# Performance work log

Hardware: AMD Instinct MI355X
Metric: run time of the kernel (lower is better)

The kernel has to match this reference:

```python
import jax, jax.numpy as jnp
import numpy as np

L = 8          # n_layer
D = 512        # hidden_size
DIN = 1024     # d_inner = 2*D (Mamba expand=2)
DS = 16        # d_state
DTR = 32       # dt_rank = ceil(D/16)
K = 4          # d_conv
NACT = 3       # n_action_to_predict
ADIM = 4
LOSS_COEF = 1.0

def silu(x):
    return x * jax.nn.sigmoid(x)

def rms(x, w, eps=1e-5):
    return x * jax.lax.rsqrt(jnp.mean(x * x, axis=-1, keepdims=True) + eps) * w

def tokenize(images, states, actions, patch_w, patch_b, state_w, state_b, act_w, act_b):
    # images [b,l,3,224,224] -> 14x14 patches of 3*16*16=768 -> mean-pooled image token
    b, l = images.shape[:2]
    p = images.reshape(b, l, 3, 14, 16, 14, 16).transpose(0, 1, 3, 5, 2, 4, 6).reshape(b, l, 196, 768)
    img = jnp.mean(p @ patch_w.T + patch_b, axis=2)            # [b,l,D] token_type 1
    st = states[:, :, 0] @ state_w.T + state_b                 # [b,l,D] token_type 2
    ac = actions[:, :, :NACT - 1] @ act_w.T + act_b            # [b,l,NACT-1,D] token_type 3
    toks = jnp.concatenate([img[:, :, None], st[:, :, None], ac], axis=2)  # [b,l,1+NACT,D]
    return toks.reshape(b, l * (1 + NACT), D)

def mamba_mixer(x, in_w, cw, cb, xpw, dtw, dtb, alog, dp, ow):
    # x: [b,S,D]
    b, S, _ = x.shape
    xz = x @ in_w.T                                   # [b,S,2*DIN]
    xi, z = xz[..., :DIN], xz[..., DIN:]
    # causal depthwise conv, kernel K
    xp = jnp.pad(xi, ((0, 0), (K - 1, 0), (0, 0)))
    xc = cb + sum(cw[:, k] * xp[:, k:k + S, :] for k in range(K))
    xc = silu(xc)
    proj = xc @ xpw.T                                  # [b,S,DTR+2*DS]
    dtr, Bm, Cm = proj[..., :DTR], proj[..., DTR:DTR + DS], proj[..., DTR + DS:]
    dt = jax.nn.softplus(dtr @ dtw.T + dtb)            # [b,S,DIN]
    A = -jnp.exp(alog)                                 # [DIN,DS]
    dA = jnp.exp(dt[..., None] * A)                    # [b,S,DIN,DS]
    dBx = dt[..., None] * Bm[:, :, None, :] * xc[..., None]
    def step(h, inp):
        a_t, bx_t = inp
        h = a_t * h + bx_t
        return h, h
    _, hs = jax.lax.scan(step, jnp.zeros((b, DIN, DS), x.dtype),
                         (dA.swapaxes(0, 1), dBx.swapaxes(0, 1)))  # hs [S,b,DIN,DS]
    y = jnp.einsum('sbdn,bsn->bsd', hs, Cm) + dp * xc
    return (y * silu(z)) @ ow.T

def _forward(images, seq_length, states, actions, action_labels,
             patch_w, patch_b, state_w, state_b, act_w, act_b,
             norm1_w, in_proj_w, conv_w, conv_b, x_proj_w, dt_w, dt_b,
             A_log, Dp, out_proj_w, norm2_w, fc1_w, fc2_w, norm_f_w,
             head_w, head_b):
    b, l = images.shape[:2]
    hidden = tokenize(images, states, actions, patch_w, patch_b, state_w, state_b, act_w, act_b)
    residual = jnp.zeros_like(hidden)
    for i in range(L):
        residual = hidden + residual
        hidden = mamba_mixer(rms(residual, norm1_w[i]), in_proj_w[i], conv_w[i], conv_b[i],
                             x_proj_w[i], dt_w[i], dt_b[i], A_log[i], Dp[i], out_proj_w[i])
        residual = hidden + residual
        g = rms(residual, norm2_w[i]) @ fc1_w[i].T       # GatedMLP fc1 -> [.., 2*DIN]
        hidden = (g[..., :DIN] * silu(g[..., DIN:])) @ fc2_w[i].T
    residual = hidden + residual
    hidden = rms(residual, norm_f_w)
    # static action-token positions: per-frame tokens [img, state, act, act] -> indices 1..3
    hs = hidden.reshape(b, l, 1 + NACT, D)[:, :, 1:, :]
    action_preds = hs @ head_w.T + head_b                # [b,l,NACT,ADIM]
    mask = (jnp.arange(l)[None, :] < seq_length[:, None]).astype(jnp.float32)
    la = jnp.mean(jnp.abs(action_preds - action_labels), axis=(2, 3))
    la = (la * mask).sum(axis=1) / jnp.clip(mask.sum(axis=1), 1.0)
    loss = jnp.mean(la) * LOSS_COEF
    return loss, action_preds

def setup_inputs() -> dict:
    key = jax.random.key(0)
    ks = iter(jax.random.split(key, 40))
    nrm = lambda shape, s=0.02: s * jax.random.normal(next(ks), shape, dtype=jnp.float32)
    inp = {
        'images': jax.random.normal(next(ks), (2, 64, 3, 224, 224), jnp.float32),
        'seq_length': jax.random.randint(next(ks), (2,), 1, 65),
        'states': jax.random.normal(next(ks), (2, 64, NACT, 7), jnp.float32),
        'actions': jax.random.normal(next(ks), (2, 64, NACT, ADIM), jnp.float32),
        'action_labels': jax.random.normal(next(ks), (2, 64, NACT, ADIM), jnp.float32),
        'patch_w': nrm((D, 768)), 'patch_b': jnp.zeros((D,), jnp.float32),
        'state_w': nrm((D, 7)), 'state_b': jnp.zeros((D,), jnp.float32),
        'act_w': nrm((D, ADIM)), 'act_b': jnp.zeros((D,), jnp.float32),
        'norm1_w': jnp.ones((L, D), jnp.float32),
        'in_proj_w': nrm((L, 2 * DIN, D)),
        'conv_w': nrm((L, DIN, K), 0.1), 'conv_b': jnp.zeros((L, DIN), jnp.float32),
        'x_proj_w': nrm((L, DTR + 2 * DS, DIN)),
        'dt_w': nrm((L, DIN, DTR)), 'dt_b': jnp.full((L, DIN), -4.6, jnp.float32),
        'A_log': jnp.log(jnp.broadcast_to(jnp.arange(1, DS + 1, dtype=jnp.float32), (L, DIN, DS))).copy(),
        'Dp': jnp.ones((L, DIN), jnp.float32),
        'out_proj_w': nrm((L, D, DIN)),
        'norm2_w': jnp.ones((L, D), jnp.float32),
        'fc1_w': nrm((L, 2 * DIN, D)), 'fc2_w': nrm((L, D, DIN)),
        'norm_f_w': jnp.ones((D,), jnp.float32),
        'head_w': nrm((ADIM, D)), 'head_b': jnp.zeros((ADIM,), jnp.float32),
    }
    return inp

def reference(images, seq_length, states, actions, action_labels,
              patch_w, patch_b, state_w, state_b, act_w, act_b,
              norm1_w, in_proj_w, conv_w, conv_b, x_proj_w, dt_w, dt_b,
              A_log, Dp, out_proj_w, norm2_w, fc1_w, fc2_w, norm_f_w,
              head_w, head_b):
    return _forward(images, seq_length, states, actions, action_labels,
                    patch_w, patch_b, state_w, state_b, act_w, act_b,
                    norm1_w, in_proj_w, conv_w, conv_b, x_proj_w, dt_w, dt_b,
                    A_log, Dp, out_proj_w, norm2_w, fc1_w, fc2_w, norm_f_w,
                    head_w, head_b)
```

## Files before the change

### kernel.cpp

```cpp
#include <hip/hip_runtime.h>


#define NTOK 512
#define SEQ  256
#define CS   32
#define NC   8

typedef __attribute__((ext_vector_type(8))) short bf16x8;
typedef __attribute__((ext_vector_type(16))) float f32x16;

__device__ __forceinline__ float silu_f(float x) { return x / (1.0f + expf(-x)); }
__device__ __forceinline__ float softplus_f(float x) {
  return (x > 20.0f) ? x : log1pf(expf(x));
}

__device__ __forceinline__ void split_pack(float4 v, uint2* hi, uint2* lo) {
  uint ux = __float_as_uint(v.x), uy = __float_as_uint(v.y);
  uint uz = __float_as_uint(v.z), uw = __float_as_uint(v.w);
  hi->x = (ux >> 16) | (uy & 0xffff0000u);
  hi->y = (uz >> 16) | (uw & 0xffff0000u);
  float lx = v.x - __uint_as_float(ux & 0xffff0000u);
  float ly = v.y - __uint_as_float(uy & 0xffff0000u);
  float lz = v.z - __uint_as_float(uz & 0xffff0000u);
  float lw = v.w - __uint_as_float(uw & 0xffff0000u);
  lo->x = (__float_as_uint(lx) >> 16) | (__float_as_uint(ly) & 0xffff0000u);
  lo->y = (__float_as_uint(lz) >> 16) | (__float_as_uint(lw) & 0xffff0000u);
}

__global__ __launch_bounds__(256) void gemm_bs_k(const float* __restrict__ A,
                                                 const float* __restrict__ B,
                                                 float* __restrict__ C,
                                                 int M, int N, int K, int Kc) {
  __shared__ alignas(16) ushort sAh[2][2][2][512];
  __shared__ alignas(16) ushort sAl[2][2][2][512];
  __shared__ alignas(16) ushort sBh[2][2][2][512];
  __shared__ alignas(16) ushort sBl[2][2][2][512];
  int t = threadIdx.x;
  int bn = blockIdx.x, bm = blockIdx.y, z = blockIdx.z;
  const float* Ab = A + (size_t)bm * 64 * K + (size_t)z * Kc;
  const float* Bb = B + (size_t)bn * 64 * K + (size_t)z * Kc;
  float* Cb = C + (size_t)z * M * N;
  int r = t >> 2, kc = (t & 3) << 2;
  int st = r >> 5, m = r & 31;
  int off = ((kc >> 3) << 8) + (m << 3) + (kc & 7);
  int w = t >> 6, lane = t & 63;
  int wr = w >> 1, wc = w & 1;

  f32x16 acc;
#pragma unroll
  for (int i = 0; i < 16; ++i) acc[i] = 0.f;

  int ns = Kc >> 5;
  const float* Ar = Ab + (size_t)r * K + kc;
  const float* Br = Bb + (size_t)r * K + kc;
  float4 a0 = *(const float4*)&Ar[0];
  float4 a1 = *(const float4*)&Ar[16];
  float4 b0 = *(const float4*)&Br[0];
  float4 b1 = *(const float4*)&Br[16];
  {
    uint2 hi, lo;
    split_pack(a0, &hi, &lo);
    *(uint2*)&sAh[0][0][st][off] = hi; *(uint2*)&sAl[0][0][st][off] = lo;
    split_pack(a1, &hi, &lo);
    *(uint2*)&sAh[0][1][st][off] = hi; *(uint2*)&sAl[0][1][st][off] = lo;
    split_pack(b0, &hi, &lo);
    *(uint2*)&sBh[0][0][st][off] = hi; *(uint2*)&sBl[0][0][st][off] = lo;
    split_pack(b1, &hi, &lo);
    *(uint2*)&sBh[0][1][st][off] = hi; *(uint2*)&sBl[0][1][st][off] = lo;
  }
  __syncthreads();
  for (int ssi = 0; ssi < ns; ++ssi) {
    int buf = ssi & 1;
    if (ssi + 1 < ns) {
      a0 = *(const float4*)&Ar[(ssi + 1) * 32];
      a1 = *(const float4*)&Ar[(ssi + 1) * 32 + 16];
      b0 = *(const float4*)&Br[(ssi + 1) * 32];
      b1 = *(const float4*)&Br[(ssi + 1) * 32 + 16];
    }
    bf16x8 ah = *(bf16x8*)&sAh[buf][0][wr][lane << 3];
    bf16x8 al = *(bf16x8*)&sAl[buf][0][wr][lane << 3];
    bf16x8 bh = *(bf16x8*)&sBh[buf][0][wc][lane << 3];
    bf16x8 bl = *(bf16x8*)&sBl[buf][0][wc][lane << 3];
    acc = __builtin_amdgcn_mfma_f32_32x32x16_bf16(ah, bh, acc, 0, 0, 0);
    acc = __builtin_amdgcn_mfma_f32_32x32x16_bf16(al, bh, acc, 0, 0, 0);
    acc = __builtin_amdgcn_mfma_f32_32x32x16_bf16(ah, bl, acc, 0, 0, 0);
    bf16x8 ah1 = *(bf16x8*)&sAh[buf][1][wr][lane << 3];
    bf16x8 al1 = *(bf16x8*)&sAl[buf][1][wr][lane << 3];
    bf16x8 bh1 = *(bf16x8*)&sBh[buf][1][wc][lane << 3];
    bf16x8 bl1 = *(bf16x8*)&sBl[buf][1][wc][lane << 3];
    acc = __builtin_amdgcn_mfma_f32_32x32x16_bf16(ah1, bh1, acc, 0, 0, 0);
    acc = __builtin_amdgcn_mfma_f32_32x32x16_bf16(al1, bh1, acc, 0, 0, 0);
    acc = __builtin_amdgcn_mfma_f32_32x32x16_bf16(ah1, bl1, acc, 0, 0, 0);
    if (ssi + 1 < ns) {
      uint2 hi, lo;
      split_pack(a0, &hi, &lo);
      *(uint2*)&sAh[buf ^ 1][0][st][off] = hi; *(uint2*)&sAl[buf ^ 1][0][st][off] = lo;
      split_pack(a1, &hi, &lo);
      *(uint2*)&sAh[buf ^ 1][1][st][off] = hi; *(uint2*)&sAl[buf ^ 1][1][st][off] = lo;
      split_pack(b0, &hi, &lo);
      *(uint2*)&sBh[buf ^ 1][0][st][off] = hi; *(uint2*)&sBl[buf ^ 1][0][st][off] = lo;
      split_pack(b1, &hi, &lo);
      *(uint2*)&sBh[buf ^ 1][1][st][off] = hi; *(uint2*)&sBl[buf ^ 1][1][st][off] = lo;
    }
    __syncthreads();
  }
  int col = lane & 31, rq = lane >> 5;
  float* Cw = Cb + (size_t)(bm * 64 + wr * 32) * N + bn * 64 + wc * 32 + col;
#pragma unroll
  for (int rg = 0; rg < 16; ++rg) {
    int row = (rg & 3) + ((rg >> 2) << 3) + (rq << 2);
    Cw[(size_t)row * N] = acc[rg];
  }
}

__global__ __launch_bounds__(256) void gemm_glu_k(const float* __restrict__ G,
                                                  const float* __restrict__ B,
                                                  float* __restrict__ C,
                                                  int M, int N, int K, int Kc) {
  __shared__ alignas(16) ushort sAh[2][2][2][512];
  __shared__ alignas(16) ushort sAl[2][2][2][512];
  __shared__ alignas(16) ushort sBh[2][2][2][512];
  __shared__ alignas(16) ushort sBl[2][2][2][512];
  int t = threadIdx.x;
  int bn = blockIdx.x, bm = blockIdx.y, z = blockIdx.z;
  const float* Gb = G + (size_t)bm * 64 * 2048 + (size_t)z * Kc;
  const float* Bb = B + (size_t)bn * 64 * K + (size_t)z * Kc;
  float* Cb = C + (size_t)z * M * N;
  int r = t >> 2, kc = (t & 3) << 2;
  int st = r >> 5, m = r & 31;
  int off = ((kc >> 3) << 8) + (m << 3) + (kc & 7);
  int w = t >> 6, lane = t & 63;
  int wr = w >> 1, wc = w & 1;

  f32x16 acc;
#pragma unroll
  for (int i = 0; i < 16; ++i) acc[i] = 0.f;

  int ns = Kc >> 5;
  const float* gr = Gb + (size_t)r * 2048 + kc;
  const float* Br = Bb + (size_t)r * K + kc;
  float4 ga0 = *(const float4*)&gr[0];
  float4 gz0 = *(const float4*)&gr[1024];
  float4 ga1 = *(const float4*)&gr[16];
  float4 gz1 = *(const float4*)&gr[1040];
  float4 b0 = *(const float4*)&Br[0];
  float4 b1 = *(const float4*)&Br[16];
  {
    float4 a0 = {ga0.x * silu_f(gz0.x), ga0.y * silu_f(gz0.y),
                 ga0.z * silu_f(gz0.z), ga0.w * silu_f(gz0.w)};
    float4 a1 = {ga1.x * silu_f(gz1.x), ga1.y * silu_f(gz1.y),
                 ga1.z * silu_f(gz1.z), ga1.w * silu_f(gz1.w)};
    uint2 hi, lo;
    split_pack(a0, &hi, &lo);
    *(uint2*)&sAh[0][0][st][off] = hi; *(uint2*)&sAl[0][0][st][off] = lo;
    split_pack(a1, &hi, &lo);
    *(uint2*)&sAh[0][1][st][off] = hi; *(uint2*)&sAl[0][1][st][off] = lo;
    split_pack(b0, &hi, &lo);
    *(uint2*)&sBh[0][0][st][off] = hi; *(uint2*)&sBl[0][0][st][off] = lo;
    split_pack(b1, &hi, &lo);
    *(uint2*)&sBh[0][1][st][off] = hi; *(uint2*)&sBl[0][1][st][off] = lo;
  }
  __syncthreads();
  for (int ssi = 0; ssi < ns; ++ssi) {
    int buf = ssi & 1;
    if (ssi + 1 < ns) {
      ga0 = *(const float4*)&gr[(ssi + 1) * 32];
      gz0 = *(const float4*)&gr[1024 + (ssi + 1) * 32];
      ga1 = *(const float4*)&gr[(ssi + 1) * 32 + 16];
      gz1 = *(const float4*)&gr[1040 + (ssi + 1) * 32];
      b0 = *(const float4*)&Br[(ssi + 1) * 32];
      b1 = *(const float4*)&Br[(ssi + 1) * 32 + 16];
    }
    bf16x8 ah = *(bf16x8*)&sAh[buf][0][wr][lane << 3];
    bf16x8 al = *(bf16x8*)&sAl[buf][0][wr][lane << 3];
    bf16x8 bh = *(bf16x8*)&sBh[buf][0][wc][lane << 3];
    bf16x8 bl = *(bf16x8*)&sBl[buf][0][wc][lane << 3];
    acc = __builtin_amdgcn_mfma_f32_32x32x16_bf16(ah, bh, acc, 0, 0, 0);
    acc = __builtin_amdgcn_mfma_f32_32x32x16_bf16(al, bh, acc, 0, 0, 0);
    acc = __builtin_amdgcn_mfma_f32_32x32x16_bf16(ah, bl, acc, 0, 0, 0);
    bf16x8 ah1 = *(bf16x8*)&sAh[buf][1][wr][lane << 3];
    bf16x8 al1 = *(bf16x8*)&sAl[buf][1][wr][lane << 3];
    bf16x8 bh1 = *(bf16x8*)&sBh[buf][1][wc][lane << 3];
    bf16x8 bl1 = *(bf16x8*)&sBl[buf][1][wc][lane << 3];
    acc = __builtin_amdgcn_mfma_f32_32x32x16_bf16(ah1, bh1, acc, 0, 0, 0);
    acc = __builtin_amdgcn_mfma_f32_32x32x16_bf16(al1, bh1, acc, 0, 0, 0);
    acc = __builtin_amdgcn_mfma_f32_32x32x16_bf16(ah1, bl1, acc, 0, 0, 0);
    if (ssi + 1 < ns) {
      float4 a0 = {ga0.x * silu_f(gz0.x), ga0.y * silu_f(gz0.y),
                   ga0.z * silu_f(gz0.z), ga0.w * silu_f(gz0.w)};
      float4 a1 = {ga1.x * silu_f(gz1.x), ga1.y * silu_f(gz1.y),
                   ga1.z * silu_f(gz1.z), ga1.w * silu_f(gz1.w)};
      uint2 hi, lo;
      split_pack(a0, &hi, &lo);
      *(uint2*)&sAh[buf ^ 1][0][st][off] = hi; *(uint2*)&sAl[buf ^ 1][0][st][off] = lo;
      split_pack(a1, &hi, &lo);
      *(uint2*)&sAh[buf ^ 1][1][st][off] = hi; *(uint2*)&sAl[buf ^ 1][1][st][off] = lo;
      split_pack(b0, &hi, &lo);
      *(uint2*)&sBh[buf ^ 1][0][st][off] = hi; *(uint2*)&sBl[buf ^ 1][0][st][off] = lo;
      split_pack(b1, &hi, &lo);
      *(uint2*)&sBh[buf ^ 1][1][st][off] = hi; *(uint2*)&sBl[buf ^ 1][1][st][off] = lo;
    }
    __syncthreads();
  }
  int col = lane & 31, rq = lane >> 5;
  float* Cw = Cb + (size_t)(bm * 64 + wr * 32) * N + bn * 64 + wc * 32 + col;
#pragma unroll
  for (int rg = 0; rg < 16; ++rg) {
    int row = (rg & 3) + ((rg >> 2) << 3) + (rq << 2);
    Cw[(size_t)row * N] = acc[rg];
  }
}

__global__ void patch_part_k(const float* __restrict__ img, float* __restrict__ pmp) {
  int blk = blockIdx.x;
  int bl = blk / 14, hb = blk % 14;
  int t = threadIdx.x;
  int c = t >> 6, hi = (t >> 2) & 15, wi4 = t & 3;
  const float* base = img + (size_t)bl * 3 * 50176 + (size_t)c * 50176 +
                      (size_t)(hb * 16 + hi) * 224 + wi4 * 4;
  float4 s = {0.f, 0.f, 0.f, 0.f};
#pragma unroll
  for (int wb = 0; wb < 14; ++wb) {
    float4 v = *(const float4*)&base[wb * 16];
    s.x += v.x; s.y += v.y; s.z += v.z; s.w += v.w;
  }
  ((float4*)(pmp + (size_t)blk * 768))[t] = s;
}

__global__ void patch_red_k(const float* __restrict__ pmp, float* __restrict__ meanp) {
  int bl = blockIdx.x;
  int t = threadIdx.x;
  float4 s = {0.f, 0.f, 0.f, 0.f};
  for (int hb = 0; hb < 14; ++hb) {
    float4 v = ((const float4*)(pmp + (size_t)(bl * 14 + hb) * 768))[t];
    s.x += v.x; s.y += v.y; s.z += v.z; s.w += v.w;
  }
  const float inv = 1.0f / 196.0f;
  float4 o = {s.x * inv, s.y * inv, s.z * inv, s.w * inv};
  ((float4*)(meanp + (size_t)bl * 768))[t] = o;
}

__global__ void tokenize_k(const float* __restrict__ imgp,
                           const float* __restrict__ states,
                           const float* __restrict__ actions,
                           const float* __restrict__ pb,
                           const float* __restrict__ sw, const float* __restrict__ sb,
                           const float* __restrict__ aw, const float* __restrict__ ab,
                           float* __restrict__ hidden, float* __restrict__ residual) {
  int tok = blockIdx.x;
  int t = threadIdx.x;
  int j = tok & 3;
  int bl = tok >> 2;
  int o0 = t * 4;
  float out[4];
  if (j == 0) {
    float4 a = ((const float4*)pb)[t];
    const float* ip = imgp + (size_t)bl * 512;
#pragma unroll
    for (int p = 0; p < 8; ++p) {
      float4 v = ((const float4*)(ip + (size_t)p * 65536))[t];
      a.x += v.x; a.y += v.y; a.z += v.z; a.w += v.w;
    }
    out[0] = a.x; out[1] = a.y; out[2] = a.z; out[3] = a.w;
  } else if (j == 1) {
    const float* sv = states + (size_t)bl * 21;
#pragma unroll
    for (int i = 0; i < 4; ++i) {
      int o = o0 + i;
      float acc = sb[o];
      for (int k = 0; k < 7; ++k) acc += sw[o * 7 + k] * sv[k];
      out[i] = acc;
    }
  } else {
    const float* av = actions + ((size_t)bl * 3 + (j - 2)) * 4;
#pragma unroll
    for (int i = 0; i < 4; ++i) {
      int o = o0 + i;
      float acc = ab[o];
      for (int k = 0; k < 4; ++k) acc += aw[o * 4 + k] * av[k];
      out[i] = acc;
    }
  }
  float4 ov = {out[0], out[1], out[2], out[3]};
  ((float4*)(hidden + (size_t)tok * 512))[t] = ov;
  float4 z4 = {0.f, 0.f, 0.f, 0.f};
  ((float4*)(residual + (size_t)tok * 512))[t] = z4;
}

__global__ void addnorm_k(const float* __restrict__ hid, int parts,
                          float* __restrict__ res,
                          const float* __restrict__ w, float* __restrict__ xn) {
  int tok = blockIdx.x;
  int t = threadIdx.x;
  float4* r4 = (float4*)(res + (size_t)tok * 512);
  float4 r = r4[t];
  const float4* hp = (const float4*)(hid + (size_t)tok * 512);
  for (int p = 0; p < parts; ++p) {
    float4 h = hp[t];
    r.x += h.x; r.y += h.y; r.z += h.z; r.w += h.w;
    hp += 65536;
  }
  r4[t] = r;
  float ss = r.x * r.x + r.y * r.y + r.z * r.z + r.w * r.w;
  for (int off = 32; off; off >>= 1) ss += __shfl_down(ss, off, 64);
  __shared__ float s2[2];
  if ((t & 63) == 0) s2[t >> 6] = ss;
  __syncthreads();
  float tot = s2[0] + s2[1];
  float scale = rsqrtf(tot * (1.0f / 512.0f) + 1e-5f);
  float4 wv = ((const float4*)w)[t];
  float4 o = {r.x * scale * wv.x, r.y * scale * wv.y,
              r.z * scale * wv.z, r.w * scale * wv.w};
  ((float4*)(xn + (size_t)tok * 512))[t] = o;
}

__global__ __launch_bounds__(256) void convproj_k(const float* __restrict__ xz,
                                                  const float* __restrict__ cw,
                                                  const float* __restrict__ cb,
                                                  const float* __restrict__ xpw,
                                                  const float* __restrict__ dtw,
                                                  const float* __restrict__ dtbias,
                                                  float* __restrict__ xc,
                                                  float* __restrict__ proj,
                                                  float* __restrict__ dt) {
  int tok = blockIdx.x;
  int t = threadIdx.x;
  int b = tok >> 8, s = tok & 255;
  __shared__ float xr[1024];
  __shared__ float pp[4][64];
  __shared__ float pr[64];
  int d4 = t * 4;
  float4 cw0 = ((const float4*)cw)[d4];
  float4 cw1 = ((const float4*)cw)[d4 + 1];
  float4 cw2 = ((const float4*)cw)[d4 + 2];
  float4 cw3 = ((const float4*)cw)[d4 + 3];
  float acc0 = cb[d4], acc1 = cb[d4 + 1], acc2 = cb[d4 + 2], acc3 = cb[d4 + 3];
  const float* base = xz + (size_t)b * 256 * 2048 + d4;
  const float wk0[4] = {cw0.x, cw0.y, cw0.z, cw0.w};
  const float wk1[4] = {cw1.x, cw1.y, cw1.z, cw1.w};
  const float wk2[4] = {cw2.x, cw2.y, cw2.z, cw2.w};
  const float wk3[4] = {cw3.x, cw3.y, cw3.z, cw3.w};
#pragma unroll
  for (int k = 0; k < 4; ++k) {
    int row = s + k - 3;
    if (row >= 0) {
      float4 v = *(const float4*)&base[(size_t)row * 2048];
      acc0 += wk0[k] * v.x; acc1 += wk1[k] * v.y;
      acc2 += wk2[k] * v.z; acc3 += wk3[k] * v.w;
    }
  }
  float4 xc4 = {silu_f(acc0), silu_f(acc1), silu_f(acc2), silu_f(acc3)};
  ((float4*)(xc + (size_t)tok * 1024))[t] = xc4;
  *(float4*)&xr[d4] = xc4;
  __syncthreads();
  int n = t & 63, q = t >> 6;
  {
    const float* wrow = xpw + (size_t)n * 1024 + q * 256;
    const float* xq = xr + q * 256;
    float acc = 0.f;
    for (int k = 0; k < 256; k += 4)
      acc += wrow[k] * xq[k] + wrow[k + 1] * xq[k + 1] +
             wrow[k + 2] * xq[k + 2] + wrow[k + 3] * xq[k + 3];
    pp[q][n] = acc;
  }
  __syncthreads();
  if (t < 64) {
    float v = pp[0][t] + pp[1][t] + pp[2][t] + pp[3][t];
    pr[t] = v;
    proj[(size_t)tok * 64 + t] = v;
  }
  __syncthreads();
#pragma unroll
  for (int i = 0; i < 4; ++i) {
    int d = t * 4 + i;
    const float* dw = dtw + (size_t)d * 32;
    float a = dtbias[d];
    for (int k = 0; k < 32; ++k) a += dw[k] * pr[k];
    dt[(size_t)tok * 1024 + d] = softplus_f(a);
  }
}

__global__ __launch_bounds__(512) void scan_k(const float* __restrict__ dt,
                                              const float* __restrict__ proj,
                                              const float* __restrict__ xc,
                                              const float* __restrict__ xz,
                                              const float* __restrict__ alog,
                                              const float* __restrict__ Dp,
                                              float* __restrict__ yz) {
  __shared__ float sDt[256][4];
  __shared__ float sXc[256][4];
  __shared__ float sZ[256][4];
  __shared__ float sBC[256][32];
  __shared__ float2 sP[8][4][16];
  __shared__ float sY[256][4];
  int t = threadIdx.x;
  int g = blockIdx.x;
  int b = g >> 8;
  int d0 = (g & 255) << 2;
  int c = t >> 6, dl = (t >> 4) & 3, n = t & 15;
  int d = d0 + dl;
  const float* dtb = dt + (size_t)b * 256 * 1024 + d0;
  const float* xcb = xc + (size_t)b * 256 * 1024 + d0;
  const float* zb  = xz + (size_t)b * 256 * 2048 + 1024 + d0;
  const float* pbp = proj + (size_t)b * 256 * 64 + 32;
  float* yb = yz + (size_t)b * 256 * 1024 + d0;

  if (t < 256) {
    *(float4*)&sDt[t][0] = *(const float4*)&dtb[(size_t)t * 1024];
    *(float4*)&sZ[t][0]  = *(const float4*)&zb[(size_t)t * 2048];
  } else {
    int u = t - 256;
    *(float4*)&sXc[u][0] = *(const float4*)&xcb[(size_t)u * 1024];
  }
#pragma unroll
  for (int i = 0; i < 4; ++i) {
    int idx = i * 512 + t;
    int s = idx >> 3, c4 = (idx & 7) << 2;
    *(float4*)&sBC[s][c4] = *(const float4*)&pbp[(size_t)s * 64 + c4];
  }
  float A = -expf(alog[d * 16 + n]);
  float dp = Dp[d];
  __syncthreads();

  float Ap = 1.f, Bacc = 0.f;
#pragma unroll
  for (int i = 0; i < CS; ++i) {
    int s = (c << 5) + i;
    float dtv = sDt[s][dl];
    float dA = __expf(dtv * A);
    Bacc = dA * Bacc + dtv * sBC[s][n] * sXc[s][dl];
    Ap *= dA;
  }
  sP[c][dl][n] = make_float2(Ap, Bacc);
  __syncthreads();

  float h = 0.f;
  for (int cc = 0; cc < c; ++cc) {
    float2 p = sP[cc][dl][n];
    h = p.x * h + p.y;
  }

#pragma unroll
  for (int i = 0; i < CS; ++i) {
    int s = (c << 5) + i;
    float dtv = sDt[s][dl];
    float xcv = sXc[s][dl];
    float dA = __expf(dtv * A);
    h = dA * h + dtv * sBC[s][n] * xcv;
    float yc = h * sBC[s][16 + n];
    yc += __shfl_xor(yc, 1, 64);
    yc += __shfl_xor(yc, 2, 64);
    yc += __shfl_xor(yc, 4, 64);
    yc += __shfl_xor(yc, 8, 64);
    if (n == 0) sY[s][dl] = (yc + dp * xcv) * silu_f(sZ[s][dl]);
  }
  __syncthreads();
  if (t < 256)
    *(float4*)&yb[(size_t)t * 1024] = *(const float4*)&sY[t][0];
}

__global__ void head_k(const float* __restrict__ hf, const float* __restrict__ hw,
                       const float* __restrict__ hb, const float* __restrict__ labels,
                       float* __restrict__ preds, float* __restrict__ labs) {
  int blk = blockIdx.x;
  int j = blk % 3;
  int l = (blk / 3) % 64;
  int b = blk / 192;
  int row = b * 256 + l * 4 + 1 + j;
  int t = threadIdx.x;
  const float* x = hf + (size_t)row * 512;
  float acc[4] = {0.f, 0.f, 0.f, 0.f};
  for (int k = t; k < 512; k += 64) {
    float xv = x[k];
#pragma unroll
    for (int a = 0; a < 4; ++a) acc[a] += xv * hw[a * 512 + k];
  }
  for (int off = 32; off; off >>= 1) {
#pragma unroll
    for (int a = 0; a < 4; ++a) acc[a] += __shfl_down(acc[a], off, 64);
  }
  if (t == 0) {
    const float* lab = labels + (size_t)blk * 4;
    float sd = 0.f;
#pragma unroll
    for (int a = 0; a < 4; ++a) {
      float p = acc[a] + hb[a];
      preds[(size_t)blk * 4 + a] = p;
      sd += fabsf(p - lab[a]);
    }
    labs[blk] = sd;
  }
}

__global__ void loss_k(const float* __restrict__ labs, const int* __restrict__ seqlen,
                       float* __restrict__ out) {
  int t = threadIdx.x;
  int b = t >> 6, l = t & 63;
  float la = (labs[(b * 64 + l) * 3] + labs[(b * 64 + l) * 3 + 1] +
              labs[(b * 64 + l) * 3 + 2]) * (1.0f / 12.0f);
  float m = (l < seqlen[b]) ? 1.f : 0.f;
  float v = la * m;
  for (int off = 32; off; off >>= 1) {
    v += __shfl_down(v, off, 64);
    m += __shfl_down(m, off, 64);
  }
  __shared__ float sb_[2];
  if ((t & 63) == 0) sb_[b] = v / fmaxf(m, 1.0f);
  __syncthreads();
  if (t == 0) out[0] = 0.5f * (sb_[0] + sb_[1]);
}

extern "C" void kernel_launch(void* const* d_in, const int* in_sizes, int n_in,
                              void* d_out, int out_size, void* d_ws, size_t ws_size,
                              hipStream_t stream) {
  const float* images     = (const float*)d_in[0];
  const int*   seq_length = (const int*)d_in[1];
  const float* states     = (const float*)d_in[2];
  const float* actions    = (const float*)d_in[3];
  const float* labels     = (const float*)d_in[4];
  const float* patch_w    = (const float*)d_in[5];
  const float* patch_b    = (const float*)d_in[6];
  const float* state_w    = (const float*)d_in[7];
  const float* state_b    = (const float*)d_in[8];
  const float* act_w      = (const float*)d_in[9];
  const float* act_b      = (const float*)d_in[10];
  const float* norm1_w    = (const float*)d_in[11];
  const float* in_proj_w  = (const float*)d_in[12];
  const float* conv_w     = (const float*)d_in[13];
  const float* conv_b     = (const float*)d_in[14];
  const float* x_proj_w   = (const float*)d_in[15];
  const float* dt_w       = (const float*)d_in[16];
  const float* dt_b       = (const float*)d_in[17];
  const float* A_log      = (const float*)d_in[18];
  const float* Dp         = (const float*)d_in[19];
  const float* out_proj_w = (const float*)d_in[20];
  const float* norm2_w    = (const float*)d_in[21];
  const float* fc1_w      = (const float*)d_in[22];
  const float* fc2_w      = (const float*)d_in[23];
  const float* norm_f_w   = (const float*)d_in[24];
  const float* head_w     = (const float*)d_in[25];
  const float* head_b     = (const float*)d_in[26];

  float* out = (float*)d_out;

  float* ws = (float*)d_ws;
  float* meanp    = ws; ws += 98304;
  float* hidden   = ws; ws += 262144;
  float* residual = ws; ws += 262144;
  float* xn       = ws; ws += 262144;
  float* xz       = ws; ws += 1048576;
  float* xc       = ws; ws += 524288;
  float* proj     = ws; ws += 32768;
  float* dtbuf    = ws; ws += 524288;
  float* yz       = ws; ws += 524288;
  float* labs     = ws; ws += 384;
  float* cpart    = ws; ws += 1048576;
  float* pmp      = ws; ws += 1376256;

  hipLaunchKernelGGL(patch_part_k, dim3(1792), dim3(192), 0, stream, images, pmp);
  hipLaunchKernelGGL(patch_red_k, dim3(128), dim3(192), 0, stream, pmp, meanp);
  hipLaunchKernelGGL(gemm_bs_k, dim3(8, 2, 8), dim3(256), 0, stream,
                     meanp, patch_w, cpart, 128, 512, 768, 96);
  hipLaunchKernelGGL(tokenize_k, dim3(512), dim3(128), 0, stream, cpart, states, actions,
                     patch_b, state_w, state_b, act_w, act_b, hidden, residual);

  for (int i = 0; i < 8; ++i) {
    const float* n1 = norm1_w + i * 512;
    const float* ipw = in_proj_w + (size_t)i * 2048 * 512;
    const float* cw = conv_w + (size_t)i * 4096;
    const float* cb = conv_b + (size_t)i * 1024;
    const float* xpw = x_proj_w + (size_t)i * 65536;
    const float* dtw = dt_w + (size_t)i * 32768;
    const float* dtbias = dt_b + (size_t)i * 1024;
    const float* al = A_log + (size_t)i * 16384;
    const float* dpp = Dp + (size_t)i * 1024;
    const float* opw = out_proj_w + (size_t)i * 524288;
    const float* n2 = norm2_w + i * 512;
    const float* f1 = fc1_w + (size_t)i * 1048576;
    const float* f2 = fc2_w + (size_t)i * 524288;

    if (i == 0)
      hipLaunchKernelGGL(addnorm_k, dim3(512), dim3(128), 0, stream,
                         hidden, 1, residual, n1, xn);
    else
      hipLaunchKernelGGL(addnorm_k, dim3(512), dim3(128), 0, stream,
                         cpart, 4, residual, n1, xn);
    hipLaunchKernelGGL(gemm_bs_k, dim3(32, 8, 1), dim3(256), 0, stream,
                       xn, ipw, xz, 512, 2048, 512, 512);
    hipLaunchKernelGGL(convproj_k, dim3(512), dim3(256), 0, stream,
                       xz, cw, cb, xpw, dtw, dtbias, xc, proj, dtbuf);
    hipLaunchKernelGGL(scan_k, dim3(512), dim3(512), 0, stream,
                       dtbuf, proj, xc, xz, al, dpp, yz);
    hipLaunchKernelGGL(gemm_bs_k, dim3(8, 8, 4), dim3(256), 0, stream,
                       yz, opw, cpart, 512, 512, 1024, 256);
    hipLaunchKernelGGL(addnorm_k, dim3(512), dim3(128), 0, stream,
                       cpart, 4, residual, n2, xn);
    hipLaunchKernelGGL(gemm_bs_k, dim3(32, 8, 1), dim3(256), 0, stream,
                       xn, f1, xz, 512, 2048, 512, 512);
    hipLaunchKernelGGL(gemm_glu_k, dim3(8, 8, 4), dim3(256), 0, stream,
                       xz, f2, cpart, 512, 512, 1024, 256);
  }

  hipLaunchKernelGGL(addnorm_k, dim3(512), dim3(128), 0, stream,
                     cpart, 4, residual, norm_f_w, xn);
  hipLaunchKernelGGL(head_k, dim3(384), dim3(64), 0, stream, xn, head_w, head_b, labels,
                     out + 1, labs);
  hipLaunchKernelGGL(loss_k, dim3(1), dim3(128), 0, stream, labs, seq_length, out);
}
```

Baseline: 1.117 ms.

## Fuse RMSNorm into GEMM prologues and residual add into GEMM epilogues

Removes the standalone addnorm kernels. The in_proj and fc1 GEMMs now compute each row's RMS scale from the residual themselves and apply the norm weight while staging tiles. The out_proj and fc2 GEMMs drop split-K and add their results directly into the residual buffer. Patch pooling collapses into one kernel, and the final norm folds into the head kernel. This cuts launches and intermediate traffic, but the RMW GEMMs now launch only 64 blocks with serial K, which lowers parallelism, and every norm-fused GEMM block recomputes the row norm.

```diff
diff --git a/kernel.cpp b/kernel.cpp
--- a/kernel.cpp
+++ b/kernel.cpp
@@ -4,7 +4,6 @@
 #define NTOK 512
 #define SEQ  256
 #define CS   32
-#define NC   8
 
 typedef __attribute__((ext_vector_type(8))) short bf16x8;
 typedef __attribute__((ext_vector_type(16))) float f32x16;
@@ -113,19 +112,126 @@
   }
 }
 
-__global__ __launch_bounds__(256) void gemm_glu_k(const float* __restrict__ G,
-                                                  const float* __restrict__ B,
-                                                  float* __restrict__ C,
-                                                  int M, int N, int K, int Kc) {
+__global__ __launch_bounds__(256) void gemm_an_k(const float* __restrict__ res,
+                                                 const float* __restrict__ nw,
+                                                 const float* __restrict__ B,
+                                                 float* __restrict__ C, int N) {
   __shared__ alignas(16) ushort sAh[2][2][2][512];
   __shared__ alignas(16) ushort sAl[2][2][2][512];
   __shared__ alignas(16) ushort sBh[2][2][2][512];
   __shared__ alignas(16) ushort sBl[2][2][2][512];
-  int t = threadIdx.x;
-  int bn = blockIdx.x, bm = blockIdx.y, z = blockIdx.z;
-  const float* Gb = G + (size_t)bm * 64 * 2048 + (size_t)z * Kc;
-  const float* Bb = B + (size_t)bn * 64 * K + (size_t)z * Kc;
-  float* Cb = C + (size_t)z * M * N;
+  __shared__ float snw[512];
+  int t = threadIdx.x;
+  int bn = blockIdx.x, bm = blockIdx.y;
+  int r = t >> 2, kc = (t & 3) << 2;
+  int row = bm * 64 + r;
+  int st = r >> 5, m = r & 31;
+  int off = ((kc >> 3) << 8) + (m << 3) + (kc & 7);
+  int w = t >> 6, lane = t & 63;
+  int wr = w >> 1, wc = w & 1;
+
+  if (t < 128) *(float4*)&snw[t * 4] = *(const float4*)&nw[t * 4];
+
+  const float* rp = res + (size_t)row * 512;
+  float ss = 0.f;
+#pragma unroll 8
+  for (int j = 0; j < 32; ++j) {
+    float4 v = *(const float4*)&rp[((t & 3) << 2) + j * 16];
+    ss += v.x * v.x + v.y * v.y + v.z * v.z + v.w * v.w;
+  }
+  ss += __shfl_xor(ss, 1, 64);
+  ss += __shfl_xor(ss, 2, 64);
+  float scale = rsqrtf(ss * (1.0f / 512.0f) + 1e-5f);
+  __syncthreads();
+
+  f32x16 acc;
+#pragma unroll
+  for (int i = 0; i < 16; ++i) acc[i] = 0.f;
+
+  const float* Ar = rp + kc;
+  const float* Br = B + (size_t)(bn * 64 + r) * 512 + kc;
+  float4 a0 = *(const float4*)&Ar[0];
+  float4 a1 = *(const float4*)&Ar[16];
+  float4 b0 = *(const float4*)&Br[0];
+  float4 b1 = *(const float4*)&Br[16];
+  {
+    float4 w0 = *(const float4*)&snw[kc];
+    float4 w1 = *(const float4*)&snw[kc + 16];
+    float4 p0 = {a0.x * scale * w0.x, a0.y * scale * w0.y,
+                 a0.z * scale * w0.z, a0.w * scale * w0.w};
+    float4 p1 = {a1.x * scale * w1.x, a1.y * scale * w1.y,
+                 a1.z * scale * w1.z, a1.w * scale * w1.w};
+    uint2 hi, lo;
+    split_pack(p0, &hi, &lo);
+    *(uint2*)&sAh[0][0][st][off] = hi; *(uint2*)&sAl[0][0][st][off] = lo;
+    split_pack(p1, &hi, &lo);
+    *(uint2*)&sAh[0][1][st][off] = hi; *(uint2*)&sAl[0][1][st][off] = lo;
+    split_pack(b0, &hi, &lo);
+    *(uint2*)&sBh[0][0][st][off] = hi; *(uint2*)&sBl[0][0][st][off] = lo;
+    split_pack(b1, &hi, &lo);
+    *(uint2*)&sBh[0][1][st][off] = hi; *(uint2*)&sBl[0][1][st][off] = lo;
+  }
+  __syncthreads();
+  for (int ssi = 0; ssi < 16; ++ssi) {
+    int buf = ssi & 1;
+    if (ssi + 1 < 16) {
+      a0 = *(const float4*)&Ar[(ssi + 1) * 32];
+      a1 = *(const float4*)&Ar[(ssi + 1) * 32 + 16];
+      b0 = *(const float4*)&Br[(ssi + 1) * 32];
+      b1 = *(const float4*)&Br[(ssi + 1) * 32 + 16];
+    }
+    bf16x8 ah = *(bf16x8*)&sAh[buf][0][wr][lane << 3];
+    bf16x8 al = *(bf16x8*)&sAl[buf][0][wr][lane << 3];
+    bf16x8 bh = *(bf16x8*)&sBh[buf][0][wc][lane << 3];
+    bf16x8 bl = *(bf16x8*)&sBl[buf][0][wc][lane << 3];
+    acc = __builtin_amdgcn_mfma_f32_32x32x16_bf16(ah, bh, acc, 0, 0, 0);
+    acc = __builtin_amdgcn_mfma_f32_32x32x16_bf16(al, bh, acc, 0, 0, 0);
+    acc = __builtin_amdgcn_mfma_f32_32x32x16_bf16(ah, bl, acc, 0, 0, 0);
+    bf16x8 ah1 = *(bf16x8*)&sAh[buf][1][wr][lane << 3];
+    bf16x8 al1 = *(bf16x8*)&sAl[buf][1][wr][lane << 3];
+    bf16x8 bh1 = *(bf16x8*)&sBh[buf][1][wc][lane << 3];
+    bf16x8 bl1 = *(bf16x8*)&sBl[buf][1][wc][lane << 3];
+    acc = __builtin_amdgcn_mfma_f32_32x32x16_bf16(ah1, bh1, acc, 0, 0, 0);
+    acc = __builtin_amdgcn_mfma_f32_32x32x16_bf16(al1, bh1, acc, 0, 0, 0);
+    acc = __builtin_amdgcn_mfma_f32_32x32x16_bf16(ah1, bl1, acc, 0, 0, 0);
+    if (ssi + 1 < 16) {
+      int c0 = (ssi + 1) * 32 + kc;
+      float4 w0 = *(const float4*)&snw[c0];
+      float4 w1 = *(const float4*)&snw[c0 + 16];
+      float4 p0 = {a0.x * scale * w0.x, a0.y * scale * w0.y,
+                   a0.z * scale * w0.z, a0.w * scale * w0.w};
+      float4 p1 = {a1.x * scale * w1.x, a1.y * scale * w1.y,
+                   a1.z * scale * w1.z, a1.w * scale * w1.w};
+      uint2 hi, lo;
+      split_pack(p0, &hi, &lo);
+      *(uint2*)&sAh[buf ^ 1][0][st][off] = hi; *(uint2*)&sAl[buf ^ 1][0][st][off] = lo;
+      split_pack(p1, &hi, &lo);
+      *(uint2*)&sAh[buf ^ 1][1][st][off] = hi; *(uint2*)&sAl[buf ^ 1][1][st][off] = lo;
+      split_pack(b0, &hi, &lo);
+      *(uint2*)&sBh[buf ^ 1][0][st][off] = hi; *(uint2*)&sBl[buf ^ 1][0][st][off] = lo;
+      split_pack(b1, &hi, &lo);
+      *(uint2*)&sBh[buf ^ 1][1][st][off] = hi; *(uint2*)&sBl[buf ^ 1][1][st][off] = lo;
+    }
+    __syncthreads();
+  }
+  int col = lane & 31, rq = lane >> 5;
+  float* Cw = C + (size_t)(bm * 64 + wr * 32) * N + bn * 64 + wc * 32 + col;
+#pragma unroll
+  for (int rg = 0; rg < 16; ++rg) {
+    int row2 = (rg & 3) + ((rg >> 2) << 3) + (rq << 2);
+    Cw[(size_t)row2 * N] = acc[rg];
+  }
+}
+
+__global__ __launch_bounds__(256) void gemm_rmw_k(const float* __restrict__ A,
+                                                  const float* __restrict__ B,
+                                                  float* __restrict__ resid) {
+  __shared__ alignas(16) ushort sAh[2][2][2][512];
+  __shared__ alignas(16) ushort sAl[2][2][2][512];
+  __shared__ alignas(16) ushort sBh[2][2][2][512];
+  __shared__ alignas(16) ushort sBl[2][2][2][512];
+  int t = threadIdx.x;
+  int bn = blockIdx.x, bm = blockIdx.y;
   int r = t >> 2, kc = (t & 3) << 2;
   int st = r >> 5, m = r & 31;
   int off = ((kc >> 3) << 8) + (m << 3) + (kc & 7);
@@ -136,9 +242,89 @@
 #pragma unroll
   for (int i = 0; i < 16; ++i) acc[i] = 0.f;
 
-  int ns = Kc >> 5;
-  const float* gr = Gb + (size_t)r * 2048 + kc;
-  const float* Br = Bb + (size_t)r * K + kc;
+  const float* Ar = A + (size_t)(bm * 64 + r) * 1024 + kc;
+  const float* Br = B + (size_t)(bn * 64 + r) * 1024 + kc;
+  float4 a0 = *(const float4*)&Ar[0];
+  float4 a1 = *(const float4*)&Ar[16];
+  float4 b0 = *(const float4*)&Br[0];
+  float4 b1 = *(const float4*)&Br[16];
+  {
+    uint2 hi, lo;
+    split_pack(a0, &hi, &lo);
+    *(uint2*)&sAh[0][0][st][off] = hi; *(uint2*)&sAl[0][0][st][off] = lo;
+    split_pack(a1, &hi, &lo);
+    *(uint2*)&sAh[0][1][st][off] = hi; *(uint2*)&sAl[0][1][st][off] = lo;
+    split_pack(b0, &hi, &lo);
+    *(uint2*)&sBh[0][0][st][off] = hi; *(uint2*)&sBl[0][0][st][off] = lo;
+    split_pack(b1, &hi, &lo);
+    *(uint2*)&sBh[0][1][st][off] = hi; *(uint2*)&sBl[0][1][st][off] = lo;
+  }
+  __syncthreads();
+  for (int ssi = 0; ssi < 32; ++ssi) {
+    int buf = ssi & 1;
+    if (ssi + 1 < 32) {
+      a0 = *(const float4*)&Ar[(ssi + 1) * 32];
+      a1 = *(const float4*)&Ar[(ssi + 1) * 32 + 16];
+      b0 = *(const float4*)&Br[(ssi + 1) * 32];
+      b1 = *(const float4*)&Br[(ssi + 1) * 32 + 16];
+    }
+    bf16x8 ah = *(bf16x8*)&sAh[buf][0][wr][lane << 3];
+    bf16x8 al = *(bf16x8*)&sAl[buf][0][wr][lane << 3];
+    bf16x8 bh = *(bf16x8*)&sBh[buf][0][wc][lane << 3];
+    bf16x8 bl = *(bf16x8*)&sBl[buf][0][wc][lane << 3];
+    acc = __builtin_amdgcn_mfma_f32_32x32x16_bf16(ah, bh, acc, 0, 0, 0);
+    acc = __builtin_amdgcn_mfma_f32_32x32x16_bf16(al, bh, acc, 0, 0, 0);
+    acc = __builtin_amdgcn_mfma_f32_32x32x16_bf16(ah, bl, acc, 0, 0, 0);
+    bf16x8 ah1 = *(bf16x8*)&sAh[buf][1][wr][lane << 3];
+    bf16x8 al1 = *(bf16x8*)&sAl[buf][1][wr][lane << 3];
+    bf16x8 bh1 = *(bf16x8*)&sBh[buf][1][wc][lane << 3];
+    bf16x8 bl1 = *(bf16x8*)&sBl[buf][1][wc][lane << 3];
+    acc = __builtin_amdgcn_mfma_f32_32x32x16_bf16(ah1, bh1, acc, 0, 0, 0);
+    acc = __builtin_amdgcn_mfma_f32_32x32x16_bf16(al1, bh1, acc, 0, 0, 0);
+    acc = __builtin_amdgcn_mfma_f32_32x32x16_bf16(ah1, bl1, acc, 0, 0, 0);
+    if (ssi + 1 < 32) {
+      uint2 hi, lo;
+      split_pack(a0, &hi, &lo);
+      *(uint2*)&sAh[buf ^ 1][0][st][off] = hi; *(uint2*)&sAl[buf ^ 1][0][st][off] = lo;
+      split_pack(a1, &hi, &lo);
+      *(uint2*)&sAh[buf ^ 1][1][st][off] = hi; *(uint2*)&sAl[buf ^ 1][1][st][off] = lo;
+      split_pack(b0, &hi, &lo);
+      *(uint2*)&sBh[buf ^ 1][0][st][off] = hi; *(uint2*)&sBl[buf ^ 1][0][st][off] = lo;
+      split_pack(b1, &hi, &lo);
+      *(uint2*)&sBh[buf ^ 1][1][st][off] = hi; *(uint2*)&sBl[buf ^ 1][1][st][off] = lo;
+    }
+    __syncthreads();
+  }
+  int col = lane & 31, rq = lane >> 5;
+  float* Cw = resid + (size_t)(bm * 64 + wr * 32) * 512 + bn * 64 + wc * 32 + col;
+#pragma unroll
+  for (int rg = 0; rg < 16; ++rg) {
+    int row = (rg & 3) + ((rg >> 2) << 3) + (rq << 2);
+    Cw[(size_t)row * 512] += acc[rg];
+  }
+}
+
+__global__ __launch_bounds__(256) void gemm_glu_rmw_k(const float* __restrict__ G,
+                                                      const float* __restrict__ B,
+                                                      float* __restrict__ resid) {
+  __shared__ alignas(16) ushort sAh[2][2][2][512];
+  __shared__ alignas(16) ushort sAl[2][2][2][512];
+  __shared__ alignas(16) ushort sBh[2][2][2][512];
+  __shared__ alignas(16) ushort sBl[2][2][2][512];
+  int t = threadIdx.x;
+  int bn = blockIdx.x, bm = blockIdx.y;
+  int r = t >> 2, kc = (t & 3) << 2;
+  int st = r >> 5, m = r & 31;
+  int off = ((kc >> 3) << 8) + (m << 3) + (kc & 7);
+  int w = t >> 6, lane = t & 63;
+  int wr = w >> 1, wc = w & 1;
+
+  f32x16 acc;
+#pragma unroll
+  for (int i = 0; i < 16; ++i) acc[i] = 0.f;
+
+  const float* gr = G + (size_t)(bm * 64 + r) * 2048 + kc;
+  const float* Br = B + (size_t)(bn * 64 + r) * 1024 + kc;
   float4 ga0 = *(const float4*)&gr[0];
   float4 gz0 = *(const float4*)&gr[1024];
   float4 ga1 = *(const float4*)&gr[16];
@@ -161,9 +347,9 @@
     *(uint2*)&sBh[0][1][st][off] = hi; *(uint2*)&sBl[0][1][st][off] = lo;
   }
   __syncthreads();
-  for (int ssi = 0; ssi < ns; ++ssi) {
+  for (int ssi = 0; ssi < 32; ++ssi) {
     int buf = ssi & 1;
-    if (ssi + 1 < ns) {
+    if (ssi + 1 < 32) {
       ga0 = *(const float4*)&gr[(ssi + 1) * 32];
       gz0 = *(const float4*)&gr[1024 + (ssi + 1) * 32];
       ga1 = *(const float4*)&gr[(ssi + 1) * 32 + 16];
@@ -185,7 +371,7 @@
     acc = __builtin_amdgcn_mfma_f32_32x32x16_bf16(ah1, bh1, acc, 0, 0, 0);
     acc = __builtin_amdgcn_mfma_f32_32x32x16_bf16(al1, bh1, acc, 0, 0, 0);
     acc = __builtin_amdgcn_mfma_f32_32x32x16_bf16(ah1, bl1, acc, 0, 0, 0);
-    if (ssi + 1 < ns) {
+    if (ssi + 1 < 32) {
       float4 a0 = {ga0.x * silu_f(gz0.x), ga0.y * silu_f(gz0.y),
                    ga0.z * silu_f(gz0.z), ga0.w * silu_f(gz0.w)};
       float4 a1 = {ga1.x * silu_f(gz1.x), ga1.y * silu_f(gz1.y),
@@ -203,37 +389,28 @@
     __syncthreads();
   }
   int col = lane & 31, rq = lane >> 5;
-  float* Cw = Cb + (size_t)(bm * 64 + wr * 32) * N + bn * 64 + wc * 32 + col;
+  float* Cw = resid + (size_t)(bm * 64 + wr * 32) * 512 + bn * 64 + wc * 32 + col;
 #pragma unroll
   for (int rg = 0; rg < 16; ++rg) {
     int row = (rg & 3) + ((rg >> 2) << 3) + (rq << 2);
-    Cw[(size_t)row * N] = acc[rg];
-  }
-}
-
-__global__ void patch_part_k(const float* __restrict__ img, float* __restrict__ pmp) {
-  int blk = blockIdx.x;
-  int bl = blk / 14, hb = blk % 14;
+    Cw[(size_t)row * 512] += acc[rg];
+  }
+}
+
+__global__ void patch_k(const float* __restrict__ img, float* __restrict__ meanp) {
+  int bl = blockIdx.x;
   int t = threadIdx.x;
   int c = t >> 6, hi = (t >> 2) & 15, wi4 = t & 3;
-  const float* base = img + (size_t)bl * 3 * 50176 + (size_t)c * 50176 +
-                      (size_t)(hb * 16 + hi) * 224 + wi4 * 4;
-  float4 s = {0.f, 0.f, 0.f, 0.f};
-#pragma unroll
-  for (int wb = 0; wb < 14; ++wb) {
-    float4 v = *(const float4*)&base[wb * 16];
-    s.x += v.x; s.y += v.y; s.z += v.z; s.w += v.w;
-  }
-  ((float4*)(pmp + (size_t)blk * 768))[t] = s;
-}
-
-__global__ void patch_red_k(const float* __restrict__ pmp, float* __restrict__ meanp) {
-  int bl = blockIdx.x;
-  int t = threadIdx.x;
+  const float* base0 = img + (size_t)bl * 3 * 50176 + (size_t)c * 50176 +
+                       (size_t)hi * 224 + wi4 * 4;
   float4 s = {0.f, 0.f, 0.f, 0.f};
   for (int hb = 0; hb < 14; ++hb) {
-    float4 v = ((const float4*)(pmp + (size_t)(bl * 14 + hb) * 768))[t];
-    s.x += v.x; s.y += v.y; s.z += v.z; s.w += v.w;
+    const float* base = base0 + (size_t)hb * 16 * 224;
+#pragma unroll
+    for (int wb = 0; wb < 14; ++wb) {
+      float4 v = *(const float4*)&base[wb * 16];
+      s.x += v.x; s.y += v.y; s.z += v.z; s.w += v.w;
+    }
   }
   const float inv = 1.0f / 196.0f;
   float4 o = {s.x * inv, s.y * inv, s.z * inv, s.w * inv};
@@ -246,7 +423,7 @@
                            const float* __restrict__ pb,
                            const float* __restrict__ sw, const float* __restrict__ sb,
                            const float* __restrict__ aw, const float* __restrict__ ab,
-                           float* __restrict__ hidden, float* __restrict__ residual) {
+                           float* __restrict__ residual) {
   int tok = blockIdx.x;
   int t = threadIdx.x;
   int j = tok & 3;
@@ -282,36 +459,7 @@
     }
   }
   float4 ov = {out[0], out[1], out[2], out[3]};
-  ((float4*)(hidden + (size_t)tok * 512))[t] = ov;
-  float4 z4 = {0.f, 0.f, 0.f, 0.f};
-  ((float4*)(residual + (size_t)tok * 512))[t] = z4;
-}
-
-__global__ void addnorm_k(const float* __restrict__ hid, int parts,
-                          float* __restrict__ res,
-                          const float* __restrict__ w, float* __restrict__ xn) {
-  int tok = blockIdx.x;
-  int t = threadIdx.x;
-  float4* r4 = (float4*)(res + (size_t)tok * 512);
-  float4 r = r4[t];
-  const float4* hp = (const float4*)(hid + (size_t)tok * 512);
-  for (int p = 0; p < parts; ++p) {
-    float4 h = hp[t];
-    r.x += h.x; r.y += h.y; r.z += h.z; r.w += h.w;
-    hp += 65536;
-  }
-  r4[t] = r;
-  float ss = r.x * r.x + r.y * r.y + r.z * r.z + r.w * r.w;
-  for (int off = 32; off; off >>= 1) ss += __shfl_down(ss, off, 64);
-  __shared__ float s2[2];
-  if ((t & 63) == 0) s2[t >> 6] = ss;
-  __syncthreads();
-  float tot = s2[0] + s2[1];
-  float scale = rsqrtf(tot * (1.0f / 512.0f) + 1e-5f);
-  float4 wv = ((const float4*)w)[t];
-  float4 o = {r.x * scale * wv.x, r.y * scale * wv.y,
-              r.z * scale * wv.z, r.w * scale * wv.w};
-  ((float4*)(xn + (size_t)tok * 512))[t] = o;
+  ((float4*)(residual + (size_t)tok * 512))[t] = ov;
 }
 
 __global__ __launch_bounds__(256) void convproj_k(const float* __restrict__ xz,
@@ -459,8 +607,9 @@
     *(float4*)&yb[(size_t)t * 1024] = *(const float4*)&sY[t][0];
 }
 
-__global__ void head_k(const float* __restrict__ hf, const float* __restrict__ hw,
-                       const float* __restrict__ hb, const float* __restrict__ labels,
+__global__ void head_k(const float* __restrict__ res, const float* __restrict__ wf,
+                       const float* __restrict__ hw, const float* __restrict__ hb,
+                       const float* __restrict__ labels,
                        float* __restrict__ preds, float* __restrict__ labs) {
   int blk = blockIdx.x;
   int j = blk % 3;
@@ -468,12 +617,26 @@
   int b = blk / 192;
   int row = b * 256 + l * 4 + 1 + j;
   int t = threadIdx.x;
-  const float* x = hf + (size_t)row * 512;
+  const float* x = res + (size_t)row * 512;
+  float4 v0 = ((const float4*)x)[t * 2];
+  float4 v1 = ((const float4*)x)[t * 2 + 1];
+  float ss = v0.x * v0.x + v0.y * v0.y + v0.z * v0.z + v0.w * v0.w +
+             v1.x * v1.x + v1.y * v1.y + v1.z * v1.z + v1.w * v1.w;
+  for (int off = 32; off; off >>= 1) ss += __shfl_down(ss, off, 64);
+  ss = __shfl(ss, 0, 64);
+  float scale = rsqrtf(ss * (1.0f / 512.0f) + 1e-5f);
+  float4 w0 = ((const float4*)wf)[t * 2];
+  float4 w1 = ((const float4*)wf)[t * 2 + 1];
+  float xn[8] = {v0.x * scale * w0.x, v0.y * scale * w0.y,
+                 v0.z * scale * w0.z, v0.w * scale * w0.w,
+                 v1.x * scale * w1.x, v1.y * scale * w1.y,
+                 v1.z * scale * w1.z, v1.w * scale * w1.w};
   float acc[4] = {0.f, 0.f, 0.f, 0.f};
-  for (int k = t; k < 512; k += 64) {
-    float xv = x[k];
-#pragma unroll
-    for (int a = 0; a < 4; ++a) acc[a] += xv * hw[a * 512 + k];
+#pragma unroll
+  for (int a = 0; a < 4; ++a) {
+    const float* hr = hw + (size_t)a * 512 + t * 8;
+#pragma unroll
+    for (int i = 0; i < 8; ++i) acc[a] += xn[i] * hr[i];
   }
   for (int off = 32; off; off >>= 1) {
 #pragma unroll
@@ -545,9 +708,7 @@
 
   float* ws = (float*)d_ws;
   float* meanp    = ws; ws += 98304;
-  float* hidden   = ws; ws += 262144;
   float* residual = ws; ws += 262144;
-  float* xn       = ws; ws += 262144;
   float* xz       = ws; ws += 1048576;
   float* xc       = ws; ws += 524288;
   float* proj     = ws; ws += 32768;
@@ -555,14 +716,12 @@
   float* yz       = ws; ws += 524288;
   float* labs     = ws; ws += 384;
   float* cpart    = ws; ws += 1048576;
-  float* pmp      = ws; ws += 1376256;
-
-  hipLaunchKernelGGL(patch_part_k, dim3(1792), dim3(192), 0, stream, images, pmp);
-  hipLaunchKernelGGL(patch_red_k, dim3(128), dim3(192), 0, stream, pmp, meanp);
+
+  hipLaunchKernelGGL(patch_k, dim3(128), dim3(192), 0, stream, images, meanp);
   hipLaunchKernelGGL(gemm_bs_k, dim3(8, 2, 8), dim3(256), 0, stream,
                      meanp, patch_w, cpart, 128, 512, 768, 96);
   hipLaunchKernelGGL(tokenize_k, dim3(512), dim3(128), 0, stream, cpart, states, actions,
-                     patch_b, state_w, state_b, act_w, act_b, hidden, residual);
+                     patch_b, state_w, state_b, act_w, act_b, residual);
 
   for (int i = 0; i < 8; ++i) {
     const float* n1 = norm1_w + i * 512;
@@ -579,31 +738,21 @@
     const float* f1 = fc1_w + (size_t)i * 1048576;
     const float* f2 = fc2_w + (size_t)i * 524288;
 
-    if (i == 0)
-      hipLaunchKernelGGL(addnorm_k, dim3(512), dim3(128), 0, stream,
-                         hidden, 1, residual, n1, xn);
-    else
-      hipLaunchKernelGGL(addnorm_k, dim3(512), dim3(128), 0, stream,
-                         cpart, 4, residual, n1, xn);
-    hipLaunchKernelGGL(gemm_bs_k, dim3(32, 8, 1), dim3(256), 0, stream,
-                       xn, ipw, xz, 512, 2048, 512, 512);
+    hipLaunchKernelGGL(gemm_an_k, dim3(32, 8), dim3(256), 0, stream,
+                       residual, n1, ipw, xz, 2048);
     hipLaunchKernelGGL(convproj_k, dim3(512), dim3(256), 0, stream,
                        xz, cw, cb, xpw, dtw, dtbias, xc, proj, dtbuf);
     hipLaunchKernelGGL(scan_k, dim3(512), dim3(512), 0, stream,
                        dtbuf, proj, xc, xz, al, dpp, yz);
-    hipLaunchKernelGGL(gemm_bs_k, dim3(8, 8, 4), dim3(256), 0, stream,
-                       yz, opw, cpart, 512, 512, 1024, 256);
-    hipLaunchKernelGGL(addnorm_k, dim3(512), dim3(128), 0, stream,
-                       cpart, 4, residual, n2, xn);
-    hipLaunchKernelGGL(gemm_bs_k, dim3(32, 8, 1), dim3(256), 0, stream,
-                       xn, f1, xz, 512, 2048, 512, 512);
-    hipLaunchKernelGGL(gemm_glu_k, dim3(8, 8, 4), dim3(256), 0, stream,
-                       xz, f2, cpart, 512, 512, 1024, 256);
-  }
-
-  hipLaunchKernelGGL(addnorm_k, dim3(512), dim3(128), 0, stream,
-                     cpart, 4, residual, norm_f_w, xn);
-  hipLaunchKernelGGL(head_k, dim3(384), dim3(64), 0, stream, xn, head_w, head_b, labels,
-                     out + 1, labs);
+    hipLaunchKernelGGL(gemm_rmw_k, dim3(8, 8), dim3(256), 0, stream,
+                       yz, opw, residual);
+    hipLaunchKernelGGL(gemm_an_k, dim3(32, 8), dim3(256), 0, stream,
+                       residual, n2, f1, xz, 2048);
+    hipLaunchKernelGGL(gemm_glu_rmw_k, dim3(8, 8), dim3(256), 0, stream,
+                       xz, f2, residual);
+  }
+
+  hipLaunchKernelGGL(head_k, dim3(384), dim3(64), 0, stream, residual, norm_f_w,
+                     head_w, head_b, labels, out + 1, labs);
   hipLaunchKernelGGL(loss_k, dim3(1), dim3(128), 0, stream, labs, seq_length, out);
 }
```

Measured after the change: 1.599 ms. +43.2%, slower.
